# Optimization experiments

Hardware: AMD Instinct MI355X
Metric: run time of the kernel (lower is better)

The kernel has to match this reference:

```python
import jax, jax.numpy as jnp
import numpy as np

D, H, L, FF, EPS = 3, 3, 12, 2048, 1e-5
B, C, T = 32, 2, 64


def _ln(x, g, b):
    m = jnp.mean(x, -1, keepdims=True)
    v = jnp.mean((x - m) ** 2, -1, keepdims=True)
    return (x - m) / jnp.sqrt(v + EPS) * g + b


def _mha(xq, xkv, w, b, ow, ob):
    # xq: [Tq,B,D], xkv: [S,B,D]; w: [3D,D] packed q/k/v like torch in_proj_weight
    Tq, Bb, _ = xq.shape
    S = xkv.shape[0]
    q = xq @ w[:D].T + b[:D]
    k = xkv @ w[D:2 * D].T + b[D:2 * D]
    v = xkv @ w[2 * D:].T + b[2 * D:]
    dh = D // H  # = 1
    q = q.reshape(Tq, Bb, H, dh)
    k = k.reshape(S, Bb, H, dh)
    v = v.reshape(S, Bb, H, dh)
    scores = jnp.einsum('qbhd,kbhd->bhqk', q, k) * (1.0 / np.sqrt(dh))
    att = jax.nn.softmax(scores, axis=-1)
    o = jnp.einsum('bhqk,kbhd->qbhd', att, v).reshape(Tq, Bb, D)
    return o @ ow.T + ob


def _ffn(x, w1, b1, w2, b2):
    return jax.nn.relu(x @ w1.T + b1) @ w2.T + b2


def _encode(x, p):
    def layer(h, pl):
        aw, ab, aow, aob, g1, b1, g2, b2, f1w, f1b, f2w, f2b = pl
        h = _ln(h + _mha(h, h, aw, ab, aow, aob), g1, b1)
        h = _ln(h + _ffn(h, f1w, f1b, f2w, f2b), g2, b2)
        return h, None
    h, _ = jax.lax.scan(layer, x, p)
    return h


def _decode(tgt, mem, p):
    def layer(h, pl):
        (sw, sb, sow, sob, cw, cb, cow, cob,
         g1, b1, g2, b2, g3, b3, f1w, f1b, f2w, f2b) = pl
        h = _ln(h + _mha(h, h, sw, sb, sow, sob), g1, b1)      # self-attn (no mask, as in source)
        h = _ln(h + _mha(h, mem, cw, cb, cow, cob), g2, b2)    # cross-attn
        h = _ln(h + _ffn(h, f1w, f1b, f2w, f2b), g3, b3)
        return h, None
    h, _ = jax.lax.scan(layer, tgt, p)
    return h


def _forward(src, angle, enc_p, enc_ng, enc_nb, dec_p, dec_ng, dec_nb):
    Bb, _, Tt = src.shape
    a = jnp.broadcast_to(angle.reshape(Bb, 1, 1), (Bb, 1, Tt))
    x = jnp.transpose(jnp.concatenate([src, a], axis=1), (2, 0, 1))  # [T,B,3]
    mem = _ln(_encode(x, enc_p), enc_ng, enc_nb)  # encoder memory is loop-invariant

    def dec(o):
        return _ln(_decode(o, mem, dec_p), dec_ng, dec_nb)

    out = jnp.zeros_like(x).at[0].set(x[0])

    def step(o, t):
        pred = dec(o)
        return o.at[t].set(pred[t]), None

    out, _ = jax.lax.scan(step, out, jnp.arange(1, Tt))
    return jnp.transpose(out, (1, 2, 0))  # [B,3,T]


def setup_inputs() -> dict:
    key = jax.random.key(0)
    it = iter(jax.random.split(key, 40))
    def n(shape, s=0.05):
        return jax.random.normal(next(it), shape, dtype=jnp.float32) * s
    inp = {
        'src': jax.random.normal(next(it), (B, C, T), dtype=jnp.float32),
        'angle': jax.random.normal(next(it), (B,), dtype=jnp.float32),
        'enc_attn_w': n((L, 3 * D, D)), 'enc_attn_b': n((L, 3 * D)),
        'enc_attn_ow': n((L, D, D)), 'enc_attn_ob': n((L, D)),
        'enc_ln1_g': jnp.ones((L, D)), 'enc_ln1_b': jnp.zeros((L, D)),
        'enc_ln2_g': jnp.ones((L, D)), 'enc_ln2_b': jnp.zeros((L, D)),
        'enc_ff1_w': n((L, FF, D)), 'enc_ff1_b': n((L, FF)),
        'enc_ff2_w': n((L, D, FF)), 'enc_ff2_b': n((L, D)),
        'enc_norm_g': jnp.ones((D,)), 'enc_norm_b': jnp.zeros((D,)),
        'dec_sa_w': n((L, 3 * D, D)), 'dec_sa_b': n((L, 3 * D)),
        'dec_sa_ow': n((L, D, D)), 'dec_sa_ob': n((L, D)),
        'dec_ca_w': n((L, 3 * D, D)), 'dec_ca_b': n((L, 3 * D)),
        'dec_ca_ow': n((L, D, D)), 'dec_ca_ob': n((L, D)),
        'dec_ln1_g': jnp.ones((L, D)), 'dec_ln1_b': jnp.zeros((L, D)),
        'dec_ln2_g': jnp.ones((L, D)), 'dec_ln2_b': jnp.zeros((L, D)),
        'dec_ln3_g': jnp.ones((L, D)), 'dec_ln3_b': jnp.zeros((L, D)),
        'dec_ff1_w': n((L, FF, D)), 'dec_ff1_b': n((L, FF)),
        'dec_ff2_w': n((L, D, FF)), 'dec_ff2_b': n((L, D)),
        'dec_norm_g': jnp.ones((D,)), 'dec_norm_b': jnp.zeros((D,)),
    }
    return inp


def reference(src, angle,
              enc_attn_w, enc_attn_b, enc_attn_ow, enc_attn_ob,
              enc_ln1_g, enc_ln1_b, enc_ln2_g, enc_ln2_b,
              enc_ff1_w, enc_ff1_b, enc_ff2_w, enc_ff2_b,
              enc_norm_g, enc_norm_b,
              dec_sa_w, dec_sa_b, dec_sa_ow, dec_sa_ob,
              dec_ca_w, dec_ca_b, dec_ca_ow, dec_ca_ob,
              dec_ln1_g, dec_ln1_b, dec_ln2_g, dec_ln2_b, dec_ln3_g, dec_ln3_b,
              dec_ff1_w, dec_ff1_b, dec_ff2_w, dec_ff2_b,
              dec_norm_g, dec_norm_b):
    enc_p = (enc_attn_w, enc_attn_b, enc_attn_ow, enc_attn_ob,
             enc_ln1_g, enc_ln1_b, enc_ln2_g, enc_ln2_b,
             enc_ff1_w, enc_ff1_b, enc_ff2_w, enc_ff2_b)
    dec_p = (dec_sa_w, dec_sa_b, dec_sa_ow, dec_sa_ob,
             dec_ca_w, dec_ca_b, dec_ca_ow, dec_ca_ob,
             dec_ln1_g, dec_ln1_b, dec_ln2_g, dec_ln2_b, dec_ln3_g, dec_ln3_b,
             dec_ff1_w, dec_ff1_b, dec_ff2_w, dec_ff2_b)
    return _forward(src, angle, enc_p, enc_norm_g, enc_norm_b, dec_p, dec_norm_g, dec_norm_b)
```

## Files before the change

### kernel.cpp

```cpp
#include <hip/hip_runtime.h>

#define DEV static __device__ __forceinline__

typedef _Float16 h2 __attribute__((ext_vector_type(2)));

DEV float fdot2f(h2 a, h2 b, float c) {
#if __has_builtin(__builtin_amdgcn_fdot2)
  return __builtin_amdgcn_fdot2(a, b, c, false);
#else
  return c + (float)a.x * (float)b.x + (float)a.y * (float)b.y;
#endif
}

DEV void ln3(float& a, float& b, float& c, const float* g, const float* bt) {
  float m = (a + b + c) * (1.0f / 3.0f);
  float d0 = a - m, d1 = b - m, d2 = c - m;
  float v = (d0 * d0 + d1 * d1 + d2 * d2) * (1.0f / 3.0f);
  float rs = rsqrtf(v + 1e-5f);
  a = fmaf(d0 * rs, g[0], bt[0]);
  b = fmaf(d1 * rs, g[1], bt[1]);
  c = fmaf(d2 * rs, g[2], bt[2]);
}

DEV unsigned pkh2(float a, float b) {
  h2 v = {(_Float16)a, (_Float16)b};
  return __builtin_bit_cast(unsigned, v);
}

__global__ void __launch_bounds__(256) prepack_kernel(
    const float* ea_w, const float* ea_b, const float* ea_ow, const float* ea_ob,
    const float* el1g, const float* el1b, const float* el2g, const float* el2b,
    const float* ef1w, const float* ef1b, const float* ef2w, const float* ef2b,
    const float* eng, const float* enb,
    const float* dsw, const float* dsb, const float* dsow, const float* dsob,
    const float* dcw, const float* dcb, const float* dcow, const float* dcob,
    const float* dl1g, const float* dl1b, const float* dl2g, const float* dl2b,
    const float* dl3g, const float* dl3b,
    const float* df1w, const float* df1b, const float* df2w, const float* df2b,
    const float* dng, const float* dnb,
    float* ws) {
  const int l = blockIdx.x, tid = threadIdx.x;
  const bool enc = l < 12;
  const int li = enc ? l : l - 12;
  const float* f1w = (enc ? ef1w : df1w) + li * 2048 * 3;
  const float* f1b = (enc ? ef1b : df1b) + li * 2048;
  const float* f2w = (enc ? ef2w : df2w) + li * 3 * 2048;
  uint4* FA4 = (uint4*)ws + (size_t)l * 1024;
  uint4* FB4 = (uint4*)ws + 24 * 1024 + (size_t)l * 1024;
  for (int jp = tid; jp < 1024; jp += 256) {
    const int j0 = jp * 2, j1 = j0 + 1;
    uint4 A;
    A.x = pkh2(f1w[j0 * 3 + 0], f1w[j1 * 3 + 0]);
    A.y = pkh2(f1w[j0 * 3 + 1], f1w[j1 * 3 + 1]);
    A.z = pkh2(f1w[j0 * 3 + 2], f1w[j1 * 3 + 2]);
    A.w = pkh2(f1b[j0], f1b[j1]);
    FA4[jp] = A;
    uint4 Bv;
    Bv.x = pkh2(f2w[j0], f2w[j1]);
    Bv.y = pkh2(f2w[2048 + j0], f2w[2048 + j1]);
    Bv.z = pkh2(f2w[4096 + j0], f2w[4096 + j1]);
    Bv.w = 0u;
    FB4[jp] = Bv;
  }
  float* S = ws + 196608 + l * 128;
  if (tid == 0) {
    const float* aw = (enc ? ea_w : dsw) + li * 27;
    const float* ab = (enc ? ea_b : dsb) + li * 9;
    const float* aow = (enc ? ea_ow : dsow) + li * 9;
    const float* aob = (enc ? ea_ob : dsob) + li * 3;
    for (int i = 0; i < 27; ++i) S[i] = aw[i];
    for (int i = 0; i < 9; ++i) S[27 + i] = ab[i];
    for (int i = 0; i < 9; ++i) S[36 + i] = aow[i];
    for (int i = 0; i < 3; ++i) S[45 + i] = aob[i];
    const float* p;
    p = (enc ? el1g : dl1g) + li * 3; for (int i = 0; i < 3; ++i) S[48 + i] = p[i];
    p = (enc ? el1b : dl1b) + li * 3; for (int i = 0; i < 3; ++i) S[51 + i] = p[i];
    p = (enc ? el2g : dl2g) + li * 3; for (int i = 0; i < 3; ++i) S[54 + i] = p[i];
    p = (enc ? el2b : dl2b) + li * 3; for (int i = 0; i < 3; ++i) S[57 + i] = p[i];
    p = (enc ? ef2b : df2b) + li * 3; for (int i = 0; i < 3; ++i) S[60 + i] = p[i];
    if (!enc) {
      const float* cw = dcw + li * 27;
      for (int i = 0; i < 9; ++i) {
        S[64 + i] = cw[i];
        S[94 + i] = cw[9 + i];
        S[106 + i] = cw[18 + i];
      }
      const float* cb = dcb + li * 9;
      for (int i = 0; i < 3; ++i) {
        S[73 + i] = cb[i];
        S[103 + i] = cb[3 + i];
        S[115 + i] = cb[6 + i];
      }
      for (int i = 0; i < 9; ++i) S[76 + i] = dcow[li * 9 + i];
      for (int i = 0; i < 3; ++i) S[85 + i] = dcob[li * 3 + i];
      p = dl3g + li * 3; for (int i = 0; i < 3; ++i) S[88 + i] = p[i];
      p = dl3b + li * 3; for (int i = 0; i < 3; ++i) S[91 + i] = p[i];
    }
  }
  if (l == 0 && tid == 1) {
    float* G = ws + 196608 + 24 * 128;
    for (int i = 0; i < 3; ++i) {
      G[i] = eng[i]; G[3 + i] = enb[i];
      G[6 + i] = dng[i]; G[9 + i] = dnb[i];
    }
  }
}

template <int NR>
DEV void ffn_core(const uint4* FA, const uint4* FB,
                  const float (&X0)[4], const float (&X1)[4], const float (&X2)[4],
                  float (&acc)[4][3], int lane) {
  h2 xd0[NR], xd1[NR], xd2[NR];
#pragma unroll
  for (int i = 0; i < NR; ++i) {
    xd0[i] = h2{(_Float16)X0[i], (_Float16)X0[i]};
    xd1[i] = h2{(_Float16)X1[i], (_Float16)X1[i]};
    xd2[i] = h2{(_Float16)X2[i], (_Float16)X2[i]};
  }
#pragma unroll
  for (int i = 0; i < NR; ++i) { acc[i][0] = 0.f; acc[i][1] = 0.f; acc[i][2] = 0.f; }
  const h2 z = {(_Float16)0, (_Float16)0};
#pragma unroll 4
  for (int kk = 0; kk < 16; ++kk) {
    const int jp = lane + (kk << 6);
    uint4 a = FA[jp];
    uint4 c = FB[jp];
    h2 wa0 = __builtin_bit_cast(h2, a.x), wa1 = __builtin_bit_cast(h2, a.y);
    h2 wa2 = __builtin_bit_cast(h2, a.z), bb = __builtin_bit_cast(h2, a.w);
    h2 wc0 = __builtin_bit_cast(h2, c.x), wc1 = __builtin_bit_cast(h2, c.y);
    h2 wc2 = __builtin_bit_cast(h2, c.z);
#pragma unroll
    for (int i = 0; i < NR; ++i) {
      h2 t = wa0 * xd0[i] + wa1 * xd1[i] + wa2 * xd2[i] + bb;
      t = __builtin_elementwise_max(t, z);
      acc[i][0] = fdot2f(wc0, t, acc[i][0]);
      acc[i][1] = fdot2f(wc1, t, acc[i][1]);
      acc[i][2] = fdot2f(wc2, t, acc[i][2]);
    }
  }
#pragma unroll
  for (int m = 1; m < 64; m <<= 1) {
#pragma unroll
    for (int i = 0; i < NR; ++i) {
      acc[i][0] += __shfl_xor(acc[i][0], m, 64);
      acc[i][1] += __shfl_xor(acc[i][1], m, 64);
      acc[i][2] += __shfl_xor(acc[i][2], m, 64);
    }
  }
}

template <bool DEC>
DEV void run_layer(const float* sm, const uint4* FA, const uint4* FB,
                   const float (*ckv)[8],
                   float (*h)[5], float (*hln)[5], float* kvq,
                   float (*p1)[25], float (*p2)[25],
                   float (*o_s)[5], const float* glob,
                   int R, int t, bool from_os, bool wpred,
                   int wave, int lane, int tid) {
  {
    const int r = tid >> 4, o = tid & 15;
    if (r < R && o <= 9) {
      float x0, x1, x2;
      if (DEC && from_os) {
        const bool real = r < t;
        x0 = real ? o_s[r][0] : 0.f;
        x1 = real ? o_s[r][1] : 0.f;
        x2 = real ? o_s[r][2] : 0.f;
      } else {
        x0 = h[r][0]; x1 = h[r][1]; x2 = h[r][2];
      }
      if (o < 9) {
        float v = fmaf(sm[o * 3], x0,
                  fmaf(sm[o * 3 + 1], x1, fmaf(sm[o * 3 + 2], x2, sm[27 + o])));
        kvq[r * 13 + o + o / 3] = v;
      } else {
        kvq[r * 13 + 7] = (DEC && r == R - 1 && t > 0) ? (float)(64 - t) : 1.0f;
        if (DEC && from_os) { h[r][0] = x0; h[r][1] = x1; h[r][2] = x2; }
      }
    }
    if (DEC && o == 9 && r >= R) kvq[r * 13 + 7] = 0.f;
  }
  __syncthreads();
  if (wave < 12) {
    const int hd = wave % 3, c = wave / 3;
    const int p0 = c * 16;
    float den = 0.f, num = 0.f;
    if (p0 < R) {
      const float q = kvq[lane * 13 + hd] * 1.44269504f;
#pragma unroll
      for (int pp = 0; pp < 16; ++pp) {
        const int p = p0 + pp;
        float e = exp2f(q * kvq[p * 13 + 4 + hd]);
        if (DEC) e *= kvq[p * 13 + 7];
        den += e;
        num = fmaf(e, kvq[p * 13 + 8 + hd], num);
      }
    }
    p1[lane][2 * wave] = den;
    p1[lane][2 * wave + 1] = num;
  }
  __syncthreads();
  if (DEC) {
    if (wave < 12) {
      const int r = lane, hd = wave % 3, c = wave / 3;
      float d0 = p1[r][0] + p1[r][6] + p1[r][12] + p1[r][18];
      float n0 = p1[r][1] + p1[r][7] + p1[r][13] + p1[r][19];
      float d1 = p1[r][2] + p1[r][8] + p1[r][14] + p1[r][20];
      float n1 = p1[r][3] + p1[r][9] + p1[r][15] + p1[r][21];
      float d2 = p1[r][4] + p1[r][10] + p1[r][16] + p1[r][22];
      float n2 = p1[r][5] + p1[r][11] + p1[r][17] + p1[r][23];
      float oh0 = __fdividef(n0, d0), oh1 = __fdividef(n1, d1), oh2 = __fdividef(n2, d2);
      float a0 = fmaf(sm[36], oh0, fmaf(sm[37], oh1, fmaf(sm[38], oh2, sm[45]))) + h[r][0];
      float a1 = fmaf(sm[39], oh0, fmaf(sm[40], oh1, fmaf(sm[41], oh2, sm[46]))) + h[r][1];
      float a2 = fmaf(sm[42], oh0, fmaf(sm[43], oh1, fmaf(sm[44], oh2, sm[47]))) + h[r][2];
      ln3(a0, a1, a2, sm + 48, sm + 51);
      if (wave == 0 && r < R) { hln[r][0] = a0; hln[r][1] = a1; hln[r][2] = a2; }
      float q = fmaf(sm[64 + hd * 3], a0,
                fmaf(sm[64 + hd * 3 + 1], a1,
                fmaf(sm[64 + hd * 3 + 2], a2, sm[73 + hd]))) * 1.44269504f;
      const int p0 = c * 16;
      float den = 0.f, num = 0.f;
#pragma unroll
      for (int pp = 0; pp < 16; ++pp) {
        const int p = p0 + pp;
        float e = exp2f(q * ckv[p][hd]);
        den += e;
        num = fmaf(e, ckv[p][3 + hd], num);
      }
      p2[r][2 * wave] = den;
      p2[r][2 * wave + 1] = num;
    }
    __syncthreads();
  }
  {
    const int nr = (wave < R) ? (1 + (R - 1 - wave) / 16) : 0;
    if (nr > 0) {
      const float(*pp)[25] = DEC ? p2 : p1;
      const float* ow = DEC ? sm + 76 : sm + 36;
      const float* ob = DEC ? sm + 85 : sm + 45;
      const float* lg = DEC ? sm + 54 : sm + 48;
      const float* lb = DEC ? sm + 57 : sm + 51;
      float X0[4], X1[4], X2[4];
#pragma unroll
      for (int i = 0; i < 4; ++i) {
        X0[i] = 0.f; X1[i] = 0.f; X2[i] = 0.f;
        if (i < nr) {
          const int rc = wave + 16 * i;
          float d0 = pp[rc][0] + pp[rc][6] + pp[rc][12] + pp[rc][18];
          float n0 = pp[rc][1] + pp[rc][7] + pp[rc][13] + pp[rc][19];
          float d1 = pp[rc][2] + pp[rc][8] + pp[rc][14] + pp[rc][20];
          float n1 = pp[rc][3] + pp[rc][9] + pp[rc][15] + pp[rc][21];
          float d2 = pp[rc][4] + pp[rc][10] + pp[rc][16] + pp[rc][22];
          float n2 = pp[rc][5] + pp[rc][11] + pp[rc][17] + pp[rc][23];
          float oh0 = __fdividef(n0, d0), oh1 = __fdividef(n1, d1), oh2 = __fdividef(n2, d2);
          float hr0, hr1, hr2;
          if (DEC) { hr0 = hln[rc][0]; hr1 = hln[rc][1]; hr2 = hln[rc][2]; }
          else     { hr0 = h[rc][0];   hr1 = h[rc][1];   hr2 = h[rc][2]; }
          float a0 = fmaf(ow[0], oh0, fmaf(ow[1], oh1, fmaf(ow[2], oh2, ob[0]))) + hr0;
          float a1 = fmaf(ow[3], oh0, fmaf(ow[4], oh1, fmaf(ow[5], oh2, ob[1]))) + hr1;
          float a2 = fmaf(ow[6], oh0, fmaf(ow[7], oh1, fmaf(ow[8], oh2, ob[2]))) + hr2;
          ln3(a0, a1, a2, lg, lb);
          X0[i] = a0; X1[i] = a1; X2[i] = a2;
        }
      }
      float acc[4][3];
      switch (nr) {
        case 1: ffn_core<1>(FA, FB, X0, X1, X2, acc, lane); break;
        case 2: ffn_core<2>(FA, FB, X0, X1, X2, acc, lane); break;
        case 3: ffn_core<3>(FA, FB, X0, X1, X2, acc, lane); break;
        default: ffn_core<4>(FA, FB, X0, X1, X2, acc, lane); break;
      }
      if (lane == 0) {
        const float* fg = DEC ? sm + 88 : sm + 54;
        const float* fb = DEC ? sm + 91 : sm + 57;
#pragma unroll
        for (int i = 0; i < 4; ++i) {
          if (i < nr) {
            const int r = wave + 16 * i;
            float y0 = acc[i][0] + sm[60] + X0[i];
            float y1 = acc[i][1] + sm[61] + X1[i];
            float y2 = acc[i][2] + sm[62] + X2[i];
            ln3(y0, y1, y2, fg, fb);
            h[r][0] = y0; h[r][1] = y1; h[r][2] = y2;
            if (DEC && wpred && r == R - 1) {
              ln3(y0, y1, y2, glob + 6, glob + 9);
              o_s[t][0] = y0; o_s[t][1] = y1; o_s[t][2] = y2;
            }
          }
        }
      }
    }
    __syncthreads();
  }
}

__global__ void __launch_bounds__(1024) tf_kernel(const float* src, const float* angle,
                                                  const float* ws, float* out) {
  __shared__ float small_s[24][128];
  __shared__ float glob[16];
  __shared__ float h[64][5];
  __shared__ float hln[64][5];
  __shared__ float kvq[64 * 13];
  __shared__ float part1[64][25];
  __shared__ float part2[64][25];
  __shared__ float o_s[64][5];
  __shared__ float ckcv[12][64][8];
  const int b = blockIdx.x;
  const int tid = threadIdx.x, wave = tid >> 6, lane = tid & 63;
  const uint4* FA = (const uint4*)ws;
  const uint4* FB = (const uint4*)ws + 24 * 1024;
  const float* SM = ws + 196608;
  const float* GB = SM + 24 * 128;
  for (int i = tid; i < 24 * 128; i += 1024) ((float*)small_s)[i] = SM[i];
  if (tid < 16) glob[tid] = GB[tid];
  if (tid < 64) {
    float x0 = src[b * 128 + tid];
    float x1 = src[b * 128 + 64 + tid];
    float x2 = angle[b];
    h[tid][0] = x0; h[tid][1] = x1; h[tid][2] = x2;
    o_s[tid][0] = (tid == 0) ? x0 : 0.f;
    o_s[tid][1] = (tid == 0) ? x1 : 0.f;
    o_s[tid][2] = (tid == 0) ? x2 : 0.f;
  }
  __syncthreads();
  for (int l = 0; l < 12; ++l)
    run_layer<false>(small_s[l], FA + (size_t)l * 1024, FB + (size_t)l * 1024,
                     nullptr, h, hln, kvq, part1, part2, o_s, glob,
                     64, 0, false, false, wave, lane, tid);
  if (tid < 64) {
    float a = h[tid][0], bb = h[tid][1], c = h[tid][2];
    ln3(a, bb, c, glob + 0, glob + 3);
    h[tid][0] = a; h[tid][1] = bb; h[tid][2] = c;
  }
  __syncthreads();
  if (wave < 12) {
    const float* sm = small_s[12 + wave];
    float m0 = h[lane][0], m1 = h[lane][1], m2 = h[lane][2];
    float k0 = fmaf(sm[94], m0, fmaf(sm[95], m1, fmaf(sm[96], m2, sm[103])));
    float k1 = fmaf(sm[97], m0, fmaf(sm[98], m1, fmaf(sm[99], m2, sm[104])));
    float k2 = fmaf(sm[100], m0, fmaf(sm[101], m1, fmaf(sm[102], m2, sm[105])));
    float v0 = fmaf(sm[106], m0, fmaf(sm[107], m1, fmaf(sm[108], m2, sm[115])));
    float v1 = fmaf(sm[109], m0, fmaf(sm[110], m1, fmaf(sm[111], m2, sm[116])));
    float v2 = fmaf(sm[112], m0, fmaf(sm[113], m1, fmaf(sm[114], m2, sm[117])));
    ckcv[wave][lane][0] = k0; ckcv[wave][lane][1] = k1; ckcv[wave][lane][2] = k2;
    ckcv[wave][lane][3] = v0; ckcv[wave][lane][4] = v1; ckcv[wave][lane][5] = v2;
  }
  __syncthreads();
  for (int t = 1; t < 64; ++t) {
    const int R = t + 1;
    for (int l = 0; l < 12; ++l)
      run_layer<true>(small_s[12 + l], FA + (size_t)(12 + l) * 1024,
                      FB + (size_t)(12 + l) * 1024, ckcv[l],
                      h, hln, kvq, part1, part2, o_s, glob, R, t,
                      l == 0, l == 11, wave, lane, tid);
  }
  if (tid < 192) {
    int d = tid / 64, tt = tid % 64;
    out[b * 192 + tid] = o_s[tt][d];
  }
}

extern "C" void kernel_launch(void* const* d_in, const int* in_sizes, int n_in,
                              void* d_out, int out_size, void* d_ws, size_t ws_size,
                              hipStream_t stream) {
  (void)in_sizes; (void)n_in; (void)out_size; (void)ws_size;
  float* ws = (float*)d_ws;
  prepack_kernel<<<24, 256, 0, stream>>>(
      (const float*)d_in[2], (const float*)d_in[3], (const float*)d_in[4], (const float*)d_in[5],
      (const float*)d_in[6], (const float*)d_in[7], (const float*)d_in[8], (const float*)d_in[9],
      (const float*)d_in[10], (const float*)d_in[11], (const float*)d_in[12], (const float*)d_in[13],
      (const float*)d_in[14], (const float*)d_in[15],
      (const float*)d_in[16], (const float*)d_in[17], (const float*)d_in[18], (const float*)d_in[19],
      (const float*)d_in[20], (const float*)d_in[21], (const float*)d_in[22], (const float*)d_in[23],
      (const float*)d_in[24], (const float*)d_in[25], (const float*)d_in[26], (const float*)d_in[27],
      (const float*)d_in[28], (const float*)d_in[29],
      (const float*)d_in[30], (const float*)d_in[31], (const float*)d_in[32], (const float*)d_in[33],
      (const float*)d_in[34], (const float*)d_in[35],
      ws);
  tf_kernel<<<32, 1024, 0, stream>>>((const float*)d_in[0], (const float*)d_in[1], ws,
                                     (float*)d_out);
}
```

Baseline: 6.353 ms.

## Split FFN hidden dimension across four cooperating blocks per batch with global flag sync

Launches four blocks per batch element, each computing a quarter of the 2048-wide FFN hidden dimension. The blocks exchange partial sums through global memory and wait on an atomic counter barrier before the shared residual and layernorm step. Each block still redundantly computes attention and the layernorms. This quarters the per-block FFN weight streaming and uses more CUs, but adds a cross-block spin barrier every layer (over 750 per run). It relies on all 128 blocks being co-resident, and the FFN weights are interleaved so each layer's A and B parts sit next to each other.

```diff
diff --git a/kernel.cpp b/kernel.cpp
--- a/kernel.cpp
+++ b/kernel.cpp
@@ -26,6 +26,11 @@
   h2 v = {(_Float16)a, (_Float16)b};
   return __builtin_bit_cast(unsigned, v);
 }
+
+#define WS_SM 196608
+#define WS_GLOB 199680
+#define WS_FLAGS 199696
+#define WS_GPART 199744
 
 __global__ void __launch_bounds__(256) prepack_kernel(
     const float* ea_w, const float* ea_b, const float* ea_ow, const float* ea_ob,
@@ -45,8 +50,8 @@
   const float* f1w = (enc ? ef1w : df1w) + li * 2048 * 3;
   const float* f1b = (enc ? ef1b : df1b) + li * 2048;
   const float* f2w = (enc ? ef2w : df2w) + li * 3 * 2048;
-  uint4* FA4 = (uint4*)ws + (size_t)l * 1024;
-  uint4* FB4 = (uint4*)ws + 24 * 1024 + (size_t)l * 1024;
+  uint4* FA4 = (uint4*)ws + (size_t)l * 2048;
+  uint4* FB4 = FA4 + 1024;
   for (int jp = tid; jp < 1024; jp += 256) {
     const int j0 = jp * 2, j1 = j0 + 1;
     uint4 A;
@@ -62,7 +67,8 @@
     Bv.w = 0u;
     FB4[jp] = Bv;
   }
-  float* S = ws + 196608 + l * 128;
+  if (l == 0 && tid < 32) ((int*)(ws + WS_FLAGS))[tid] = 0;
+  float* S = ws + WS_SM + l * 128;
   if (tid == 0) {
     const float* aw = (enc ? ea_w : dsw) + li * 27;
     const float* ab = (enc ? ea_b : dsb) + li * 9;
@@ -98,7 +104,7 @@
     }
   }
   if (l == 0 && tid == 1) {
-    float* G = ws + 196608 + 24 * 128;
+    float* G = ws + WS_GLOB;
     for (int i = 0; i < 3; ++i) {
       G[i] = eng[i]; G[3 + i] = enb[i];
       G[6 + i] = dng[i]; G[9 + i] = dnb[i];
@@ -107,7 +113,7 @@
 }
 
 template <int NR>
-DEV void ffn_core(const uint4* FA, const uint4* FB,
+DEV void ffn_core(const uint4* FA, int s,
                   const float (&X0)[4], const float (&X1)[4], const float (&X2)[4],
                   float (&acc)[4][3], int lane) {
   h2 xd0[NR], xd1[NR], xd2[NR];
@@ -120,11 +126,11 @@
 #pragma unroll
   for (int i = 0; i < NR; ++i) { acc[i][0] = 0.f; acc[i][1] = 0.f; acc[i][2] = 0.f; }
   const h2 z = {(_Float16)0, (_Float16)0};
-#pragma unroll 4
-  for (int kk = 0; kk < 16; ++kk) {
-    const int jp = lane + (kk << 6);
+#pragma unroll
+  for (int kk = 0; kk < 4; ++kk) {
+    const int jp = (s << 8) + lane + (kk << 6);
     uint4 a = FA[jp];
-    uint4 c = FB[jp];
+    uint4 c = FA[1024 + jp];
     h2 wa0 = __builtin_bit_cast(h2, a.x), wa1 = __builtin_bit_cast(h2, a.y);
     h2 wa2 = __builtin_bit_cast(h2, a.z), bb = __builtin_bit_cast(h2, a.w);
     h2 wc0 = __builtin_bit_cast(h2, c.x), wc1 = __builtin_bit_cast(h2, c.y);
@@ -150,11 +156,11 @@
 }
 
 template <bool DEC>
-DEV void run_layer(const float* sm, const uint4* FA, const uint4* FB,
-                   const float (*ckv)[8],
-                   float (*h)[5], float (*hln)[5], float* kvq,
+DEV void run_layer(const float* sm, const uint4* FA, const float (*ckv)[8],
+                   float (*h)[5], float (*hln)[5], float (*xs)[5], float* kvq,
                    float (*p1)[25], float (*p2)[25],
                    float (*o_s)[5], const float* glob,
+                   float* gpart, int* flagp, int bb, int s, int cc,
                    int R, int t, bool from_os, bool wpred,
                    int wave, int lane, int tid) {
   {
@@ -261,76 +267,108 @@
           float a2 = fmaf(ow[6], oh0, fmaf(ow[7], oh1, fmaf(ow[8], oh2, ob[2]))) + hr2;
           ln3(a0, a1, a2, lg, lb);
           X0[i] = a0; X1[i] = a1; X2[i] = a2;
+          if (lane == 0) { xs[rc][0] = a0; xs[rc][1] = a1; xs[rc][2] = a2; }
         }
       }
       float acc[4][3];
       switch (nr) {
-        case 1: ffn_core<1>(FA, FB, X0, X1, X2, acc, lane); break;
-        case 2: ffn_core<2>(FA, FB, X0, X1, X2, acc, lane); break;
-        case 3: ffn_core<3>(FA, FB, X0, X1, X2, acc, lane); break;
-        default: ffn_core<4>(FA, FB, X0, X1, X2, acc, lane); break;
+        case 1: ffn_core<1>(FA, s, X0, X1, X2, acc, lane); break;
+        case 2: ffn_core<2>(FA, s, X0, X1, X2, acc, lane); break;
+        case 3: ffn_core<3>(FA, s, X0, X1, X2, acc, lane); break;
+        default: ffn_core<4>(FA, s, X0, X1, X2, acc, lane); break;
       }
       if (lane == 0) {
-        const float* fg = DEC ? sm + 88 : sm + 54;
-        const float* fb = DEC ? sm + 91 : sm + 57;
 #pragma unroll
         for (int i = 0; i < 4; ++i) {
           if (i < nr) {
             const int r = wave + 16 * i;
-            float y0 = acc[i][0] + sm[60] + X0[i];
-            float y1 = acc[i][1] + sm[61] + X1[i];
-            float y2 = acc[i][2] + sm[62] + X2[i];
-            ln3(y0, y1, y2, fg, fb);
-            h[r][0] = y0; h[r][1] = y1; h[r][2] = y2;
-            if (DEC && wpred && r == R - 1) {
-              ln3(y0, y1, y2, glob + 6, glob + 9);
-              o_s[t][0] = y0; o_s[t][1] = y1; o_s[t][2] = y2;
-            }
+            float* gp = gpart + (((size_t)(cc & 1) * 32 + bb) * 4 + s) * 256 + r * 4;
+            __hip_atomic_store(gp + 0, acc[i][0], __ATOMIC_RELAXED, __HIP_MEMORY_SCOPE_AGENT);
+            __hip_atomic_store(gp + 1, acc[i][1], __ATOMIC_RELAXED, __HIP_MEMORY_SCOPE_AGENT);
+            __hip_atomic_store(gp + 2, acc[i][2], __ATOMIC_RELAXED, __HIP_MEMORY_SCOPE_AGENT);
           }
         }
       }
     }
     __syncthreads();
   }
+  if (tid == 0) {
+    __threadfence();
+    __hip_atomic_fetch_add(flagp, 1, __ATOMIC_RELEASE, __HIP_MEMORY_SCOPE_AGENT);
+    const int target = 4 * cc;
+    while (__hip_atomic_load(flagp, __ATOMIC_ACQUIRE, __HIP_MEMORY_SCOPE_AGENT) < target) {
+      __builtin_amdgcn_s_sleep(1);
+    }
+  }
+  __syncthreads();
+  if (wave == 0 && lane < R) {
+    const int r = lane;
+    float y0 = sm[60], y1 = sm[61], y2 = sm[62];
+#pragma unroll
+    for (int ss = 0; ss < 4; ++ss) {
+      const float* gp = gpart + (((size_t)(cc & 1) * 32 + bb) * 4 + ss) * 256 + r * 4;
+      y0 += __hip_atomic_load(gp + 0, __ATOMIC_RELAXED, __HIP_MEMORY_SCOPE_AGENT);
+      y1 += __hip_atomic_load(gp + 1, __ATOMIC_RELAXED, __HIP_MEMORY_SCOPE_AGENT);
+      y2 += __hip_atomic_load(gp + 2, __ATOMIC_RELAXED, __HIP_MEMORY_SCOPE_AGENT);
+    }
+    y0 += xs[r][0]; y1 += xs[r][1]; y2 += xs[r][2];
+    const float* fg = DEC ? sm + 88 : sm + 54;
+    const float* fb = DEC ? sm + 91 : sm + 57;
+    ln3(y0, y1, y2, fg, fb);
+    h[r][0] = y0; h[r][1] = y1; h[r][2] = y2;
+    if (DEC && wpred && r == R - 1) {
+      ln3(y0, y1, y2, glob + 6, glob + 9);
+      o_s[t][0] = y0; o_s[t][1] = y1; o_s[t][2] = y2;
+    }
+  }
+  __syncthreads();
 }
 
 __global__ void __launch_bounds__(1024) tf_kernel(const float* src, const float* angle,
-                                                  const float* ws, float* out) {
+                                                  float* ws, float* out) {
   __shared__ float small_s[24][128];
   __shared__ float glob[16];
   __shared__ float h[64][5];
   __shared__ float hln[64][5];
+  __shared__ float xs[64][5];
   __shared__ float kvq[64 * 13];
-  __shared__ float part1[64][25];
-  __shared__ float part2[64][25];
+  __shared__ float p1[64][25];
+  __shared__ float p2[64][25];
   __shared__ float o_s[64][5];
   __shared__ float ckcv[12][64][8];
-  const int b = blockIdx.x;
+  const int g = blockIdx.x;
+  const int s = (g >> 3) & 3;
+  const int bb = (g & 7) + 8 * (g >> 5);
   const int tid = threadIdx.x, wave = tid >> 6, lane = tid & 63;
-  const uint4* FA = (const uint4*)ws;
-  const uint4* FB = (const uint4*)ws + 24 * 1024;
-  const float* SM = ws + 196608;
-  const float* GB = SM + 24 * 128;
+  const uint4* FABg = (const uint4*)ws;
+  const float* SM = ws + WS_SM;
+  const float* GB = ws + WS_GLOB;
+  float* gpart = ws + WS_GPART;
+  int* flagp = (int*)(ws + WS_FLAGS) + bb;
   for (int i = tid; i < 24 * 128; i += 1024) ((float*)small_s)[i] = SM[i];
   if (tid < 16) glob[tid] = GB[tid];
   if (tid < 64) {
-    float x0 = src[b * 128 + tid];
-    float x1 = src[b * 128 + 64 + tid];
-    float x2 = angle[b];
+    float x0 = src[bb * 128 + tid];
+    float x1 = src[bb * 128 + 64 + tid];
+    float x2 = angle[bb];
     h[tid][0] = x0; h[tid][1] = x1; h[tid][2] = x2;
     o_s[tid][0] = (tid == 0) ? x0 : 0.f;
     o_s[tid][1] = (tid == 0) ? x1 : 0.f;
     o_s[tid][2] = (tid == 0) ? x2 : 0.f;
   }
   __syncthreads();
-  for (int l = 0; l < 12; ++l)
-    run_layer<false>(small_s[l], FA + (size_t)l * 1024, FB + (size_t)l * 1024,
-                     nullptr, h, hln, kvq, part1, part2, o_s, glob,
+  int cc = 0;
+  for (int l = 0; l < 12; ++l) {
+    ++cc;
+    run_layer<false>(small_s[l], FABg + (size_t)l * 2048, nullptr,
+                     h, hln, xs, kvq, p1, p2, o_s, glob,
+                     gpart, flagp, bb, s, cc,
                      64, 0, false, false, wave, lane, tid);
+  }
   if (tid < 64) {
-    float a = h[tid][0], bb = h[tid][1], c = h[tid][2];
-    ln3(a, bb, c, glob + 0, glob + 3);
-    h[tid][0] = a; h[tid][1] = bb; h[tid][2] = c;
+    float a = h[tid][0], b2 = h[tid][1], c = h[tid][2];
+    ln3(a, b2, c, glob + 0, glob + 3);
+    h[tid][0] = a; h[tid][1] = b2; h[tid][2] = c;
   }
   __syncthreads();
   if (wave < 12) {
@@ -348,15 +386,18 @@
   __syncthreads();
   for (int t = 1; t < 64; ++t) {
     const int R = t + 1;
-    for (int l = 0; l < 12; ++l)
-      run_layer<true>(small_s[12 + l], FA + (size_t)(12 + l) * 1024,
-                      FB + (size_t)(12 + l) * 1024, ckcv[l],
-                      h, hln, kvq, part1, part2, o_s, glob, R, t,
-                      l == 0, l == 11, wave, lane, tid);
-  }
-  if (tid < 192) {
+    for (int li = 0; li < 12; ++li) {
+      ++cc;
+      run_layer<true>(small_s[12 + li], FABg + (size_t)(12 + li) * 2048,
+                      (const float(*)[8])ckcv[li],
+                      h, hln, xs, kvq, p1, p2, o_s, glob,
+                      gpart, flagp, bb, s, cc, R, t,
+                      li == 0, li == 11, wave, lane, tid);
+    }
+  }
+  if (s == 0 && tid < 192) {
     int d = tid / 64, tt = tid % 64;
-    out[b * 192 + tid] = o_s[tt][d];
+    out[bb * 192 + tid] = o_s[tt][d];
   }
 }
 
@@ -377,6 +418,6 @@
       (const float*)d_in[30], (const float*)d_in[31], (const float*)d_in[32], (const float*)d_in[33],
       (const float*)d_in[34], (const float*)d_in[35],
       ws);
-  tf_kernel<<<32, 1024, 0, stream>>>((const float*)d_in[0], (const float*)d_in[1], ws,
-                                     (float*)d_out);
-}
+  tf_kernel<<<128, 1024, 0, stream>>>((const float*)d_in[0], (const float*)d_in[1], ws,
+                                      (float*)d_out);
+}
```

Measured after the change: 6.743 ms. +6.1%, slower.

## Fuse next-layer QKV projection into FFN epilogue and prefetch weights early

Applied to the files above, without the earlier changes.

The FFN epilogue now computes the next layer's q/k/v projections directly from the LayerNorm output, so the separate projection phase and its barrier are skipped for every layer except the first in each pass. The first two FFN weight tiles are loaded into registers at layer entry, ahead of the attention phase, to hide global-memory latency. The FA and FB arrays are interleaved per layer for locality. This adds register pressure, and the whole wave now computes the LN values instead of only lane 0.

```diff
diff --git a/kernel.cpp b/kernel.cpp
--- a/kernel.cpp
+++ b/kernel.cpp
@@ -45,8 +45,8 @@
   const float* f1w = (enc ? ef1w : df1w) + li * 2048 * 3;
   const float* f1b = (enc ? ef1b : df1b) + li * 2048;
   const float* f2w = (enc ? ef2w : df2w) + li * 3 * 2048;
-  uint4* FA4 = (uint4*)ws + (size_t)l * 1024;
-  uint4* FB4 = (uint4*)ws + 24 * 1024 + (size_t)l * 1024;
+  uint4* FA4 = (uint4*)ws + (size_t)l * 2048;
+  uint4* FB4 = FA4 + 1024;
   for (int jp = tid; jp < 1024; jp += 256) {
     const int j0 = jp * 2, j1 = j0 + 1;
     uint4 A;
@@ -107,7 +107,7 @@
 }
 
 template <int NR>
-DEV void ffn_core(const uint4* FA, const uint4* FB,
+DEV void ffn_core(const uint4* FA, uint4 pa0, uint4 pc0, uint4 pa1, uint4 pc1,
                   const float (&X0)[4], const float (&X1)[4], const float (&X2)[4],
                   float (&acc)[4][3], int lane) {
   h2 xd0[NR], xd1[NR], xd2[NR];
@@ -120,11 +120,7 @@
 #pragma unroll
   for (int i = 0; i < NR; ++i) { acc[i][0] = 0.f; acc[i][1] = 0.f; acc[i][2] = 0.f; }
   const h2 z = {(_Float16)0, (_Float16)0};
-#pragma unroll 4
-  for (int kk = 0; kk < 16; ++kk) {
-    const int jp = lane + (kk << 6);
-    uint4 a = FA[jp];
-    uint4 c = FB[jp];
+  auto step = [&](uint4 a, uint4 c) {
     h2 wa0 = __builtin_bit_cast(h2, a.x), wa1 = __builtin_bit_cast(h2, a.y);
     h2 wa2 = __builtin_bit_cast(h2, a.z), bb = __builtin_bit_cast(h2, a.w);
     h2 wc0 = __builtin_bit_cast(h2, c.x), wc1 = __builtin_bit_cast(h2, c.y);
@@ -137,6 +133,13 @@
       acc[i][1] = fdot2f(wc1, t, acc[i][1]);
       acc[i][2] = fdot2f(wc2, t, acc[i][2]);
     }
+  };
+  step(pa0, pc0);
+  step(pa1, pc1);
+#pragma unroll 4
+  for (int kk = 2; kk < 16; ++kk) {
+    const int jp = lane + (kk << 6);
+    step(FA[jp], FA[1024 + jp]);
   }
 #pragma unroll
   for (int m = 1; m < 64; m <<= 1) {
@@ -150,14 +153,16 @@
 }
 
 template <bool DEC>
-DEV void run_layer(const float* sm, const uint4* FA, const uint4* FB,
+DEV void run_layer(const float* sm, const float* smn, const uint4* FA,
                    const float (*ckv)[8],
                    float (*h)[5], float (*hln)[5], float* kvq,
                    float (*p1)[25], float (*p2)[25],
                    float (*o_s)[5], const float* glob,
-                   int R, int t, bool from_os, bool wpred,
+                   int R, int t, bool do_p1, bool from_os, bool wpred,
                    int wave, int lane, int tid) {
-  {
+  uint4 pa0 = FA[lane], pc0 = FA[1024 + lane];
+  uint4 pa1 = FA[64 + lane], pc1 = FA[1024 + 64 + lane];
+  if (do_p1) {
     const int r = tid >> 4, o = tid & 15;
     if (r < R && o <= 9) {
       float x0, x1, x2;
@@ -179,8 +184,8 @@
       }
     }
     if (DEC && o == 9 && r >= R) kvq[r * 13 + 7] = 0.f;
-  }
-  __syncthreads();
+    __syncthreads();
+  }
   if (wave < 12) {
     const int hd = wave % 3, c = wave / 3;
     const int p0 = c * 16;
@@ -265,27 +270,34 @@
       }
       float acc[4][3];
       switch (nr) {
-        case 1: ffn_core<1>(FA, FB, X0, X1, X2, acc, lane); break;
-        case 2: ffn_core<2>(FA, FB, X0, X1, X2, acc, lane); break;
-        case 3: ffn_core<3>(FA, FB, X0, X1, X2, acc, lane); break;
-        default: ffn_core<4>(FA, FB, X0, X1, X2, acc, lane); break;
-      }
-      if (lane == 0) {
-        const float* fg = DEC ? sm + 88 : sm + 54;
-        const float* fb = DEC ? sm + 91 : sm + 57;
-#pragma unroll
-        for (int i = 0; i < 4; ++i) {
-          if (i < nr) {
-            const int r = wave + 16 * i;
-            float y0 = acc[i][0] + sm[60] + X0[i];
-            float y1 = acc[i][1] + sm[61] + X1[i];
-            float y2 = acc[i][2] + sm[62] + X2[i];
-            ln3(y0, y1, y2, fg, fb);
+        case 1: ffn_core<1>(FA, pa0, pc0, pa1, pc1, X0, X1, X2, acc, lane); break;
+        case 2: ffn_core<2>(FA, pa0, pc0, pa1, pc1, X0, X1, X2, acc, lane); break;
+        case 3: ffn_core<3>(FA, pa0, pc0, pa1, pc1, X0, X1, X2, acc, lane); break;
+        default: ffn_core<4>(FA, pa0, pc0, pa1, pc1, X0, X1, X2, acc, lane); break;
+      }
+      const float* fg = DEC ? sm + 88 : sm + 54;
+      const float* fb = DEC ? sm + 91 : sm + 57;
+#pragma unroll
+      for (int i = 0; i < 4; ++i) {
+        if (i < nr) {
+          const int r = wave + 16 * i;
+          float y0 = acc[i][0] + sm[60] + X0[i];
+          float y1 = acc[i][1] + sm[61] + X1[i];
+          float y2 = acc[i][2] + sm[62] + X2[i];
+          ln3(y0, y1, y2, fg, fb);
+          if (lane == 0) {
             h[r][0] = y0; h[r][1] = y1; h[r][2] = y2;
             if (DEC && wpred && r == R - 1) {
-              ln3(y0, y1, y2, glob + 6, glob + 9);
-              o_s[t][0] = y0; o_s[t][1] = y1; o_s[t][2] = y2;
+              float z0 = y0, z1 = y1, z2 = y2;
+              ln3(z0, z1, z2, glob + 6, glob + 9);
+              o_s[t][0] = z0; o_s[t][1] = z1; o_s[t][2] = z2;
             }
+          }
+          if (smn && lane >= 9 * i && lane < 9 * i + 9) {
+            const int o = lane - 9 * i;
+            kvq[r * 13 + o + o / 3] =
+                fmaf(smn[o * 3], y0,
+                fmaf(smn[o * 3 + 1], y1, fmaf(smn[o * 3 + 2], y2, smn[27 + o])));
           }
         }
       }
@@ -301,14 +313,13 @@
   __shared__ float h[64][5];
   __shared__ float hln[64][5];
   __shared__ float kvq[64 * 13];
-  __shared__ float part1[64][25];
-  __shared__ float part2[64][25];
+  __shared__ float p1[64][25];
+  __shared__ float p2[64][25];
   __shared__ float o_s[64][5];
   __shared__ float ckcv[12][64][8];
   const int b = blockIdx.x;
   const int tid = threadIdx.x, wave = tid >> 6, lane = tid & 63;
-  const uint4* FA = (const uint4*)ws;
-  const uint4* FB = (const uint4*)ws + 24 * 1024;
+  const uint4* FABg = (const uint4*)ws;
   const float* SM = ws + 196608;
   const float* GB = SM + 24 * 128;
   for (int i = tid; i < 24 * 128; i += 1024) ((float*)small_s)[i] = SM[i];
@@ -324,9 +335,10 @@
   }
   __syncthreads();
   for (int l = 0; l < 12; ++l)
-    run_layer<false>(small_s[l], FA + (size_t)l * 1024, FB + (size_t)l * 1024,
-                     nullptr, h, hln, kvq, part1, part2, o_s, glob,
-                     64, 0, false, false, wave, lane, tid);
+    run_layer<false>(small_s[l], (l < 11) ? small_s[l + 1] : nullptr,
+                     FABg + (size_t)l * 2048, nullptr,
+                     h, hln, kvq, p1, p2, o_s, glob,
+                     64, 0, l == 0, false, false, wave, lane, tid);
   if (tid < 64) {
     float a = h[tid][0], bb = h[tid][1], c = h[tid][2];
     ln3(a, bb, c, glob + 0, glob + 3);
@@ -348,11 +360,13 @@
   __syncthreads();
   for (int t = 1; t < 64; ++t) {
     const int R = t + 1;
-    for (int l = 0; l < 12; ++l)
-      run_layer<true>(small_s[12 + l], FA + (size_t)(12 + l) * 1024,
-                      FB + (size_t)(12 + l) * 1024, ckcv[l],
-                      h, hln, kvq, part1, part2, o_s, glob, R, t,
-                      l == 0, l == 11, wave, lane, tid);
+    for (int li = 0; li < 12; ++li)
+      run_layer<true>(small_s[12 + li], (li < 11) ? small_s[12 + li + 1] : nullptr,
+                      FABg + (size_t)(12 + li) * 2048,
+                      (const float(*)[8])ckcv[li],
+                      h, hln, kvq, p1, p2, o_s, glob, R, t,
+                      li == 0, li == 0, li == 11,
+                      wave, lane, tid);
   }
   if (tid < 192) {
     int d = tid / 64, tt = tid % 64;
```

Result: slower. 6.544 ms (+3.0%).
